# Kernel optimization log

Hardware: AMD Instinct MI355X
Metric: run time of the kernel (lower is better)

Reference implementation:

```python
import jax, jax.numpy as jnp
import numpy as np

TAU = 1.0
SCALE = 0.5
LN_EPS = 1e-5
NORM_EPS = 1e-12


def setup_inputs() -> dict:
    key = jax.random.key(0)
    k1, = jax.random.split(key, 1)
    N, D = 16384, 128
    x = jax.random.normal(k1, (N, D), dtype=jnp.float32)
    gamma = jnp.ones((D,), dtype=jnp.float32)
    beta = jnp.zeros((D,), dtype=jnp.float32)
    return {"x": x, "gamma": gamma, "beta": beta}


def reference(x, gamma, beta):
    # 'cn' branch: row-normalize, full pairwise cosine sim, row softmax, aggregate
    norm = jnp.sqrt(jnp.sum(x * x, axis=1, keepdims=True))
    norm_x = x / jnp.maximum(norm, NORM_EPS)          # [N, D]
    sim = jax.nn.softmax(norm_x @ norm_x.T / TAU, axis=1)  # [N, N]
    x_neg = sim @ x                                    # [N, D]
    y = (1.0 + SCALE) * x - SCALE * x_neg
    # LayerNorm over the hidden dim
    mu = jnp.mean(y, axis=-1, keepdims=True)
    var = jnp.mean((y - mu) ** 2, axis=-1, keepdims=True)
    return (y - mu) * jax.lax.rsqrt(var + LN_EPS) * gamma + beta
```

## Files before the change

### kernel.cpp

```cpp
#include <hip/hip_runtime.h>
#include <stdint.h>

#define NN 16384
#define DD 128
#define KT 64
#define QB 128
#define KSTR 144
#define VSTR 72
#define KBYTES 9216
#define VBYTES 9216

typedef float f32x16 __attribute__((ext_vector_type(16)));
typedef int i32x8 __attribute__((ext_vector_type(8)));

using gv = __attribute__((address_space(1))) const void;
using lv = __attribute__((address_space(3))) void;

__device__ __forceinline__ i32x8 mk8(uint4 a, uint4 b) {
  i32x8 r;
  r[0] = a.x; r[1] = a.y; r[2] = a.z; r[3] = a.w;
  r[4] = b.x; r[5] = b.y; r[6] = b.z; r[7] = b.w;
  return r;
}

#define MFMA64(A, B, C) \
  __builtin_amdgcn_mfma_scale_f32_32x32x64_f8f6f4((A), (B), (C), 0, 0, 0, 0x7F7F7F7F, 0, 0x7F7F7F7F)

__global__ void k_norm(const float* __restrict__ x, uint8_t* __restrict__ nx) {
  const int wave = threadIdx.x >> 6, lane = threadIdx.x & 63;
  const int row = blockIdx.x * 4 + wave;
  const float2 v = *reinterpret_cast<const float2*>(x + (size_t)row * DD + 2 * lane);
  float ss = v.x * v.x + v.y * v.y;
#pragma unroll
  for (int m = 1; m < 64; m <<= 1) ss += __shfl_xor(ss, m);
  const float rn = 1.2011224087f / fmaxf(sqrtf(ss), 1e-12f);
  const int w = __builtin_amdgcn_cvt_pk_fp8_f32(v.x * rn, v.y * rn, 0, false);
  *reinterpret_cast<uint16_t*>(nx + (size_t)row * DD + 2 * lane) = (uint16_t)w;
}

__global__ void k_transpose(const float* __restrict__ x, uint8_t* __restrict__ xT) {
  __shared__ uint16_t tile[64 * 66];
  const int n0 = blockIdx.x * 64;
  const int t = threadIdx.x;
#pragma unroll
  for (int e = 0; e < 16; ++e) {
    const int idx = e * 256 + t;
    const int r = idx >> 6, c2 = idx & 63;
    const float2 v = *reinterpret_cast<const float2*>(x + (size_t)(n0 + r) * DD + 2 * c2);
    const int w = __builtin_amdgcn_cvt_pk_fp8_f32(v.x, v.y, 0, false);
    tile[r * 66 + c2] = (uint16_t)w;
  }
  __syncthreads();
  const uint8_t* t8 = reinterpret_cast<const uint8_t*>(tile);
#pragma unroll
  for (int e = 0; e < 8; ++e) {
    const int idx = e * 256 + t;
    const int d = idx >> 4, n4 = (idx & 15) << 2;
    uint32_t w = (uint32_t)t8[(n4 + 0) * 132 + d];
    w |= (uint32_t)t8[(n4 + 1) * 132 + d] << 8;
    w |= (uint32_t)t8[(n4 + 2) * 132 + d] << 16;
    w |= (uint32_t)t8[(n4 + 3) * 132 + d] << 24;
    *reinterpret_cast<uint32_t*>(xT + (size_t)d * NN + n0 + n4) = w;
  }
}

template <int NSPLIT>
__global__ __launch_bounds__(256, 4) void k_attn(
    const uint8_t* __restrict__ nx, const uint8_t* __restrict__ xT,
    float* __restrict__ Op, float* __restrict__ Lp) {
  __shared__ alignas(16) uint8_t Kb[2][KBYTES];
  __shared__ alignas(16) uint8_t Vb[2][VBYTES];

  const int tid = threadIdx.x;
  const int wave = tid >> 6;
  const int lane = tid & 63;
  const int rl = lane & 31;
  const int hi = lane >> 5;

  const int id = blockIdx.x;
  constexpr int gs = 8 / NSPLIT;
  const int split = (id & 7) / gs;
  const int qblock = (id >> 3) * gs + (id & (gs - 1));

  constexpr int nt = 256 / NSPLIT;
  const int t0s = split * nt;
  const int qw = qblock * QB + wave * 32;

  const int sw = wave >> 1;
  const int j0 = (wave & 1) * 5;
  const int cnt = (wave & 1) ? 4 : 5;
  uint32_t soff[5];
#pragma unroll
  for (int i = 0; i < 5; ++i) {
    const int j = j0 + i;
    const int t16 = j * 64 + lane;
    if (sw == 0) {
      soff[i] = (uint32_t)((t16 / 9) * DD + (t16 % 9) * 16);
    } else {
      const int d = (2 * t16) / 9;
      const int c0 = t16 * 16 - d * VSTR;
      soff[i] = (uint32_t)(d * NN + c0 + (c0 >= 64 ? (NN - VSTR) : 0));
    }
  }

  auto stage = [&](int tt, int buf) {
    const int k0 = tt * KT;
    const uint8_t* basep = (sw == 0) ? (nx + (size_t)k0 * DD) : (xT + k0);
    uint8_t* ldsb = (sw == 0) ? &Kb[buf][0] : &Vb[buf][0];
#pragma unroll
    for (int i = 0; i < 5; ++i)
      if (i < cnt)
        __builtin_amdgcn_global_load_lds((gv*)(basep + soff[i]),
            (lv*)(ldsb + (j0 + i) * 1024), 16, 0, 0);
  };

  const uint8_t* qrow = nx + (size_t)(qw + rl) * DD + 32 * hi;
  i32x8 q8[2];
#pragma unroll
  for (int c = 0; c < 2; ++c)
    q8[c] = mk8(*reinterpret_cast<const uint4*>(qrow + c * 64),
                *reinterpret_cast<const uint4*>(qrow + c * 64 + 16));

  f32x16 o[4];
#pragma unroll
  for (int dt = 0; dt < 4; ++dt)
#pragma unroll
    for (int r = 0; r < 16; ++r) o[dt][r] = 0.f;
  float lsum = 0.f;

  stage(t0s, 0);

  for (int t = 0; t < nt; ++t) {
    const int buf = t & 1;
    __builtin_amdgcn_sched_barrier(0);
    asm volatile("s_waitcnt vmcnt(0)" ::: "memory");
    __builtin_amdgcn_sched_barrier(0);
    __builtin_amdgcn_s_barrier();
    __builtin_amdgcn_sched_barrier(0);
    if (t + 1 < nt) stage(t0s + t + 1, buf ^ 1);

    const uint8_t* kb = &Kb[buf][0];
    const uint8_t* vb = &Vb[buf][0];

    uint32_t W0[4], W1[4];
#pragma unroll
    for (int kt = 0; kt < 2; ++kt) {
      const uint8_t* kbb = kb + kt * 32 * KSTR + rl * KSTR + 32 * hi;
      const i32x8 ka0 = mk8(*reinterpret_cast<const uint4*>(kbb),
                            *reinterpret_cast<const uint4*>(kbb + 16));
      const i32x8 ka1 = mk8(*reinterpret_cast<const uint4*>(kbb + 64),
                            *reinterpret_cast<const uint4*>(kbb + 80));
      f32x16 s = {};
      s = MFMA64(ka0, q8[0], s);
      s = MFMA64(ka1, q8[1], s);
      float e[16];
#pragma unroll
      for (int r = 0; r < 16; ++r) {
        float p;
        asm("v_exp_f32 %0, %1" : "=v"(p) : "v"(s[r]));
        e[r] = p;
        lsum += p;
      }
      uint32_t* W = kt ? W1 : W0;
#pragma unroll
      for (int g = 0; g < 4; ++g) {
        uint32_t w = (uint32_t)__builtin_amdgcn_cvt_pk_fp8_f32(e[4 * g + 0], e[4 * g + 1], 0, false);
        w = (uint32_t)__builtin_amdgcn_cvt_pk_fp8_f32(e[4 * g + 2], e[4 * g + 3], (int)w, true);
        W[g] = w;
      }
    }
#pragma unroll
    for (int g = 0; g < 4; ++g)
      asm("v_permlane32_swap_b32 %0, %1" : "+v"(W0[g]), "+v"(W1[g]));
    i32x8 pa;
    pa[0] = (int)W0[0]; pa[1] = (int)W1[0]; pa[2] = (int)W0[1]; pa[3] = (int)W1[1];
    pa[4] = (int)W0[2]; pa[5] = (int)W1[2]; pa[6] = (int)W0[3]; pa[7] = (int)W1[3];

#pragma unroll
    for (int dt = 0; dt < 4; ++dt) {
      const uint8_t* vp = vb + (dt * 32 + rl) * VSTR + 32 * hi;
      const i32x8 vf = mk8(*reinterpret_cast<const uint4*>(vp),
                           *reinterpret_cast<const uint4*>(vp + 16));
      o[dt] = MFMA64(pa, vf, o[dt]);
    }
  }

  const float lt = lsum + __shfl_xor(lsum, 32);
  if (hi == 0) Lp[(size_t)split * NN + qw + rl] = lt;

  float* Ob = Op + (size_t)split * NN * DD;
#pragma unroll
  for (int dt = 0; dt < 4; ++dt)
#pragma unroll
    for (int r = 0; r < 16; ++r) {
      const int q = (r & 3) + 8 * (r >> 2) + 4 * hi;
      Ob[(size_t)(qw + q) * DD + dt * 32 + rl] = o[dt][r];
    }
}

__global__ void k_final(const float* __restrict__ x, const float* __restrict__ gamma,
                        const float* __restrict__ beta, const float* __restrict__ Op,
                        const float* __restrict__ Lp, float* __restrict__ out, int nsplit) {
  const int wave = threadIdx.x >> 6, lane = threadIdx.x & 63;
  const int row = blockIdx.x * 4 + wave;
  float o0 = 0.f, o1 = 0.f, lt = 0.f;
  for (int s = 0; s < nsplit; ++s) {
    const float2 v = *reinterpret_cast<const float2*>(
        Op + (size_t)s * NN * DD + (size_t)row * DD + 2 * lane);
    o0 += v.x;
    o1 += v.y;
    lt += Lp[(size_t)s * NN + row];
  }
  const float inv = 1.0f / lt;
  const float2 xv = *reinterpret_cast<const float2*>(x + (size_t)row * DD + 2 * lane);
  float y0 = 1.5f * xv.x - 0.5f * o0 * inv;
  float y1 = 1.5f * xv.y - 0.5f * o1 * inv;
  float sum = y0 + y1;
#pragma unroll
  for (int m = 1; m < 64; m <<= 1) sum += __shfl_xor(sum, m);
  const float mu = sum * (1.0f / 128.0f);
  const float d0 = y0 - mu, d1 = y1 - mu;
  float vs = d0 * d0 + d1 * d1;
#pragma unroll
  for (int m = 1; m < 64; m <<= 1) vs += __shfl_xor(vs, m);
  const float rs = rsqrtf(vs * (1.0f / 128.0f) + 1e-5f);
  const float2 g = *reinterpret_cast<const float2*>(gamma + 2 * lane);
  const float2 b = *reinterpret_cast<const float2*>(beta + 2 * lane);
  float2 ov;
  ov.x = d0 * rs * g.x + b.x;
  ov.y = d1 * rs * g.y + b.y;
  *reinterpret_cast<float2*>(out + (size_t)row * DD + 2 * lane) = ov;
}

extern "C" void kernel_launch(void* const* d_in, const int* in_sizes, int n_in,
                              void* d_out, int out_size, void* d_ws, size_t ws_size,
                              hipStream_t stream) {
  const float* x = (const float*)d_in[0];
  const float* gamma = (const float*)d_in[1];
  const float* beta = (const float*)d_in[2];
  float* out = (float*)d_out;
  char* ws = (char*)d_ws;

  uint8_t* nx = (uint8_t*)ws;
  uint8_t* xT = (uint8_t*)(ws + (size_t)NN * DD);
  const size_t base = (size_t)2 * NN * DD;
  const size_t per = (size_t)NN * DD * 4 + (size_t)NN * 4;

  int nsplit = 2;
  if (ws_size >= base + 8 * per) nsplit = 8;
  else if (ws_size >= base + 4 * per) nsplit = 4;

  float* Op = (float*)(ws + base);
  float* Lp = (float*)(ws + base + (size_t)nsplit * NN * DD * 4);

  k_norm<<<NN / 4, 256, 0, stream>>>(x, nx);
  k_transpose<<<NN / 64, 256, 0, stream>>>(x, xT);
  if (nsplit == 8)
    k_attn<8><<<dim3(128 * 8), 256, 0, stream>>>(nx, xT, Op, Lp);
  else if (nsplit == 4)
    k_attn<4><<<dim3(128 * 4), 256, 0, stream>>>(nx, xT, Op, Lp);
  else
    k_attn<2><<<dim3(128 * 2), 256, 0, stream>>>(nx, xT, Op, Lp);
  k_final<<<NN / 4, 256, 0, stream>>>(x, gamma, beta, Op, Lp, out, nsplit);
}
```

Before: 165.6 us.

## Fuse norm and transpose prep, use small fp8 MFMAs for QK, stagger tiles

Merges the row-normalize and transpose kernels into one prep kernel that reads x once and writes both the fp8 normalized rows and the fp8 transposed copy. In the attention kernel, the QK^T product switches from two scaled 32x32x64 MFMAs to eight 32x32x16 fp8 MFMAs with 8-byte operand loads. It also adds s_setprio around the MFMA sections and staggers each block's starting key tile so blocks read different K/V tiles at the same time. The exp/pack step is restructured with a pairwise lsum reduction. The risks are a higher MFMA instruction count in QK and a changed softmax summation order.

Result: slower. 193.9 us (+17.1%).

```diff
diff --git a/kernel.cpp b/kernel.cpp
--- a/kernel.cpp
+++ b/kernel.cpp
@@ -12,6 +12,7 @@
 
 typedef float f32x16 __attribute__((ext_vector_type(16)));
 typedef int i32x8 __attribute__((ext_vector_type(8)));
+typedef long long i64;
 
 using gv = __attribute__((address_space(1))) const void;
 using lv = __attribute__((address_space(3))) void;
@@ -25,44 +26,71 @@
 
 #define MFMA64(A, B, C) \
   __builtin_amdgcn_mfma_scale_f32_32x32x64_f8f6f4((A), (B), (C), 0, 0, 0, 0x7F7F7F7F, 0, 0x7F7F7F7F)
-
-__global__ void k_norm(const float* __restrict__ x, uint8_t* __restrict__ nx) {
-  const int wave = threadIdx.x >> 6, lane = threadIdx.x & 63;
-  const int row = blockIdx.x * 4 + wave;
-  const float2 v = *reinterpret_cast<const float2*>(x + (size_t)row * DD + 2 * lane);
-  float ss = v.x * v.x + v.y * v.y;
-#pragma unroll
-  for (int m = 1; m < 64; m <<= 1) ss += __shfl_xor(ss, m);
-  const float rn = 1.2011224087f / fmaxf(sqrtf(ss), 1e-12f);
-  const int w = __builtin_amdgcn_cvt_pk_fp8_f32(v.x * rn, v.y * rn, 0, false);
-  *reinterpret_cast<uint16_t*>(nx + (size_t)row * DD + 2 * lane) = (uint16_t)w;
-}
-
-__global__ void k_transpose(const float* __restrict__ x, uint8_t* __restrict__ xT) {
-  __shared__ uint16_t tile[64 * 66];
+#define LD16(p) (*reinterpret_cast<const uint4*>(p))
+
+__global__ void k_prep(const float* __restrict__ x, uint8_t* __restrict__ nx,
+                       uint8_t* __restrict__ xT) {
+  __shared__ uint8_t tile[64 * 132];
   const int n0 = blockIdx.x * 64;
   const int t = threadIdx.x;
-#pragma unroll
-  for (int e = 0; e < 16; ++e) {
-    const int idx = e * 256 + t;
-    const int r = idx >> 6, c2 = idx & 63;
-    const float2 v = *reinterpret_cast<const float2*>(x + (size_t)(n0 + r) * DD + 2 * c2);
-    const int w = __builtin_amdgcn_cvt_pk_fp8_f32(v.x, v.y, 0, false);
-    tile[r * 66 + c2] = (uint16_t)w;
-  }
+  const int r = t >> 2;
+  const int qd = t & 3;
+
+  const float* xr = x + (size_t)(n0 + r) * DD + qd * 32;
+  float4 v[8];
+  float ss = 0.f;
+#pragma unroll
+  for (int j = 0; j < 8; ++j) {
+    v[j] = *reinterpret_cast<const float4*>(xr + 4 * j);
+    ss += v[j].x * v[j].x + v[j].y * v[j].y + v[j].z * v[j].z + v[j].w * v[j].w;
+  }
+  ss += __shfl_xor(ss, 1);
+  ss += __shfl_xor(ss, 2);
+  const float rn = 1.2011224087f / fmaxf(sqrtf(ss), 1e-12f);
+
+  uint32_t nb[8];
+#pragma unroll
+  for (int j = 0; j < 8; ++j) {
+    uint32_t w = (uint32_t)__builtin_amdgcn_cvt_pk_fp8_f32(v[j].x * rn, v[j].y * rn, 0, false);
+    w = (uint32_t)__builtin_amdgcn_cvt_pk_fp8_f32(v[j].z * rn, v[j].w * rn, (int)w, true);
+    nb[j] = w;
+    uint32_t u = (uint32_t)__builtin_amdgcn_cvt_pk_fp8_f32(v[j].x, v[j].y, 0, false);
+    u = (uint32_t)__builtin_amdgcn_cvt_pk_fp8_f32(v[j].z, v[j].w, (int)u, true);
+    *reinterpret_cast<uint32_t*>(&tile[r * 132 + qd * 32 + 4 * j]) = u;
+  }
+  uint4 o0 = {nb[0], nb[1], nb[2], nb[3]};
+  uint4 o1 = {nb[4], nb[5], nb[6], nb[7]};
+  uint8_t* nrow = nx + (size_t)(n0 + r) * DD + qd * 32;
+  *reinterpret_cast<uint4*>(nrow) = o0;
+  *reinterpret_cast<uint4*>(nrow + 16) = o1;
+
   __syncthreads();
-  const uint8_t* t8 = reinterpret_cast<const uint8_t*>(tile);
 #pragma unroll
   for (int e = 0; e < 8; ++e) {
     const int idx = e * 256 + t;
     const int d = idx >> 4, n4 = (idx & 15) << 2;
-    uint32_t w = (uint32_t)t8[(n4 + 0) * 132 + d];
-    w |= (uint32_t)t8[(n4 + 1) * 132 + d] << 8;
-    w |= (uint32_t)t8[(n4 + 2) * 132 + d] << 16;
-    w |= (uint32_t)t8[(n4 + 3) * 132 + d] << 24;
+    uint32_t w = (uint32_t)tile[(n4 + 0) * 132 + d];
+    w |= (uint32_t)tile[(n4 + 1) * 132 + d] << 8;
+    w |= (uint32_t)tile[(n4 + 2) * 132 + d] << 16;
+    w |= (uint32_t)tile[(n4 + 3) * 132 + d] << 24;
     *reinterpret_cast<uint32_t*>(xT + (size_t)d * NN + n0 + n4) = w;
   }
 }
+
+#define SMPACK(sv_, W_)                                                   \
+  {                                                                       \
+    _Pragma("unroll") for (int g = 0; g < 4; ++g) {                       \
+      float e0_, e1_, e2_, e3_;                                           \
+      asm("v_exp_f32 %0, %1" : "=v"(e0_) : "v"(sv_[4 * g + 0]));          \
+      asm("v_exp_f32 %0, %1" : "=v"(e1_) : "v"(sv_[4 * g + 1]));          \
+      asm("v_exp_f32 %0, %1" : "=v"(e2_) : "v"(sv_[4 * g + 2]));          \
+      asm("v_exp_f32 %0, %1" : "=v"(e3_) : "v"(sv_[4 * g + 3]));          \
+      lsum += (e0_ + e1_) + (e2_ + e3_);                                  \
+      uint32_t w_ = (uint32_t)__builtin_amdgcn_cvt_pk_fp8_f32(e0_, e1_, 0, false); \
+      w_ = (uint32_t)__builtin_amdgcn_cvt_pk_fp8_f32(e2_, e3_, (int)w_, true);     \
+      W_[g] = w_;                                                         \
+    }                                                                     \
+  }
 
 template <int NSPLIT>
 __global__ __launch_bounds__(256, 4) void k_attn(
@@ -84,6 +112,7 @@
 
   constexpr int nt = 256 / NSPLIT;
   const int t0s = split * nt;
+  const int pst = (id >> 3) & (nt - 1);
   const int qw = qblock * QB + wave * 32;
 
   const int sw = wave >> 1;
@@ -114,12 +143,10 @@
             (lv*)(ldsb + (j0 + i) * 1024), 16, 0, 0);
   };
 
-  const uint8_t* qrow = nx + (size_t)(qw + rl) * DD + 32 * hi;
-  i32x8 q8[2];
-#pragma unroll
-  for (int c = 0; c < 2; ++c)
-    q8[c] = mk8(*reinterpret_cast<const uint4*>(qrow + c * 64),
-                *reinterpret_cast<const uint4*>(qrow + c * 64 + 16));
+  i64 q8[8];
+#pragma unroll
+  for (int dc = 0; dc < 8; ++dc)
+    q8[dc] = *reinterpret_cast<const i64*>(nx + (size_t)(qw + rl) * DD + dc * 16 + 8 * hi);
 
   f32x16 o[4];
 #pragma unroll
@@ -128,7 +155,7 @@
     for (int r = 0; r < 16; ++r) o[dt][r] = 0.f;
   float lsum = 0.f;
 
-  stage(t0s, 0);
+  stage(t0s + pst, 0);
 
   for (int t = 0; t < nt; ++t) {
     const int buf = t & 1;
@@ -137,7 +164,7 @@
     __builtin_amdgcn_sched_barrier(0);
     __builtin_amdgcn_s_barrier();
     __builtin_amdgcn_sched_barrier(0);
-    if (t + 1 < nt) stage(t0s + t + 1, buf ^ 1);
+    if (t + 1 < nt) stage(t0s + ((t + 1 + pst) & (nt - 1)), buf ^ 1);
 
     const uint8_t* kb = &Kb[buf][0];
     const uint8_t* vb = &Vb[buf][0];
@@ -145,29 +172,16 @@
     uint32_t W0[4], W1[4];
 #pragma unroll
     for (int kt = 0; kt < 2; ++kt) {
-      const uint8_t* kbb = kb + kt * 32 * KSTR + rl * KSTR + 32 * hi;
-      const i32x8 ka0 = mk8(*reinterpret_cast<const uint4*>(kbb),
-                            *reinterpret_cast<const uint4*>(kbb + 16));
-      const i32x8 ka1 = mk8(*reinterpret_cast<const uint4*>(kbb + 64),
-                            *reinterpret_cast<const uint4*>(kbb + 80));
+      const uint8_t* kbb = kb + kt * 32 * KSTR + rl * KSTR + 8 * hi;
       f32x16 s = {};
-      s = MFMA64(ka0, q8[0], s);
-      s = MFMA64(ka1, q8[1], s);
-      float e[16];
-#pragma unroll
-      for (int r = 0; r < 16; ++r) {
-        float p;
-        asm("v_exp_f32 %0, %1" : "=v"(p) : "v"(s[r]));
-        e[r] = p;
-        lsum += p;
+      __builtin_amdgcn_s_setprio(1);
+#pragma unroll
+      for (int dc = 0; dc < 8; ++dc) {
+        const i64 ka = *reinterpret_cast<const i64*>(kbb + dc * 16);
+        s = __builtin_amdgcn_mfma_f32_32x32x16_fp8_fp8(ka, q8[dc], s, 0, 0, 0);
       }
-      uint32_t* W = kt ? W1 : W0;
-#pragma unroll
-      for (int g = 0; g < 4; ++g) {
-        uint32_t w = (uint32_t)__builtin_amdgcn_cvt_pk_fp8_f32(e[4 * g + 0], e[4 * g + 1], 0, false);
-        w = (uint32_t)__builtin_amdgcn_cvt_pk_fp8_f32(e[4 * g + 2], e[4 * g + 3], (int)w, true);
-        W[g] = w;
-      }
+      __builtin_amdgcn_s_setprio(0);
+      if (kt == 0) { SMPACK(s, W0); } else { SMPACK(s, W1); }
     }
 #pragma unroll
     for (int g = 0; g < 4; ++g)
@@ -176,13 +190,14 @@
     pa[0] = (int)W0[0]; pa[1] = (int)W1[0]; pa[2] = (int)W0[1]; pa[3] = (int)W1[1];
     pa[4] = (int)W0[2]; pa[5] = (int)W1[2]; pa[6] = (int)W0[3]; pa[7] = (int)W1[3];
 
+    __builtin_amdgcn_s_setprio(1);
 #pragma unroll
     for (int dt = 0; dt < 4; ++dt) {
       const uint8_t* vp = vb + (dt * 32 + rl) * VSTR + 32 * hi;
-      const i32x8 vf = mk8(*reinterpret_cast<const uint4*>(vp),
-                           *reinterpret_cast<const uint4*>(vp + 16));
+      const i32x8 vf = mk8(LD16(vp), LD16(vp + 16));
       o[dt] = MFMA64(pa, vf, o[dt]);
     }
+    __builtin_amdgcn_s_setprio(0);
   }
 
   const float lt = lsum + __shfl_xor(lsum, 32);
@@ -253,8 +268,7 @@
   float* Op = (float*)(ws + base);
   float* Lp = (float*)(ws + base + (size_t)nsplit * NN * DD * 4);
 
-  k_norm<<<NN / 4, 256, 0, stream>>>(x, nx);
-  k_transpose<<<NN / 64, 256, 0, stream>>>(x, xT);
+  k_prep<<<NN / 64, 256, 0, stream>>>(x, nx, xT);
   if (nsplit == 8)
     k_attn<8><<<dim3(128 * 8), 256, 0, stream>>>(nx, xT, Op, Lp);
   else if (nsplit == 4)
```
